# Performance work log

Measured on AMD Instinct MI355X. Metric: run time of the kernel, lower is better.

The kernel has to match this reference:

```python
import jax, jax.numpy as jnp
import numpy as np
from jax import lax

B, T, C = 32, 512, 128
K = 3                      # top_k periods
MIN_P, MAX_P = 8, 64       # period search band
P_MAX = MAX_P              # grid width
CYC_MAX = (T + MIN_P - 1) // MIN_P
KW = 9                     # cyc-axis depthwise kernel
GN_G = 32                  # _best_gn_groups(128)
EPS_GN = 1e-5
EPS_ORTH = 1e-6
EPS_W = 1e-8


def setup_inputs() -> dict:
    key = jax.random.key(0)
    ks = jax.random.split(key, 4)
    return {
        "x": jax.random.normal(ks[0], (B, T, C), jnp.float32),
        "W_dw": jax.random.normal(ks[1], (C, 1, KW), jnp.float32) * 0.1,
        "W_pw": jax.random.normal(ks[2], (C, C), jnp.float32) * (1.0 / np.sqrt(C)),
        "gn_weight": jnp.ones((C,), jnp.float32),
        "gn_bias": jnp.zeros((C,), jnp.float32),
        "W_gate": jax.random.normal(ks[3], (C, C), jnp.float32) * (1.0 / np.sqrt(C)),
        "gamma": jnp.full((C,), 1e-3, jnp.float32),
    }


def _autocorr_topk(x):
    # x: [B,T,C] -> period idx [B,K], softmax weights [B,K]
    Xf = jnp.fft.rfft(x, axis=1)
    Pm = (Xf * jnp.conj(Xf)).real.mean(-1)          # [B, T//2+1]
    r = jnp.fft.irfft(Pm, n=T, axis=1)              # [B, T] autocorrelation
    lag = jnp.arange(T)
    valid = (lag >= MIN_P) & (lag <= MAX_P)
    very_neg = jnp.finfo(x.dtype).min / 8
    rm = jnp.where(valid[None, :], r, very_neg)
    vals, idx = lax.top_k(rm, K)
    w = jax.nn.softmax(vals, axis=1)
    return idx, w


def _fold(s, p):
    # s: [N,T,C], p: [N] int periods -> Z [N,C,CYC_MAX,P_MAX], mask, unfold index maps
    N = s.shape[0]
    p = jnp.maximum(p, 1)
    tpad = ((T + p - 1) // p) * p                   # [N]
    cyc = jnp.arange(CYC_MAX)[None, :, None]
    pos = jnp.arange(P_MAX)[None, None, :]
    time = cyc * p[:, None, None] + pos             # [N,CYC_MAX,P_MAX]
    valid = (pos < p[:, None, None]) & (time < tpad[:, None, None])
    # right-side reflect padding indices
    m = 2 * (T - 1)
    rr = time % m
    src_idx = jnp.where(rr < T, rr, m - rr)
    src = jnp.take_along_axis(s, src_idx.reshape(N, -1)[:, :, None], axis=1)
    src = src.reshape(N, CYC_MAX, P_MAX, C) * valid[..., None].astype(s.dtype)
    Z = jnp.transpose(src, (0, 3, 1, 2))            # [N,C,CYC_MAX,P_MAX]
    mask2d = valid[:, None].astype(s.dtype)         # [N,1,CYC_MAX,P_MAX]
    t = jnp.arange(T)[None, :]
    cyc_T = jnp.clip(t // p[:, None], 0, CYC_MAX - 1)
    pos_T = jnp.clip(t % p[:, None], 0, P_MAX - 1)
    return Z, mask2d, cyc_T, pos_T


def _cyc_conv(Z, mask2d, W_dw, W_pw, gn_w, gn_b, W_gate, gamma):
    # CycAxisConv1d: mean over period axis, depthwise+pointwise conv along cyc,
    # GroupNorm, GELU, SE-gate, LayerScale residual broadcast back to 2D.
    N, _, L, _ = Z.shape
    u = Z.mean(-1)                                  # [N,C,L]
    h = lax.conv_general_dilated(u, W_dw, (1,), [(KW // 2, KW // 2)],
                                 dimension_numbers=('NCH', 'OIH', 'NCH'),
                                 feature_group_count=C)
    h = jnp.einsum('oc,ncl->nol', W_pw, h)
    hg = h.reshape(N, GN_G, C // GN_G, L)
    mean = hg.mean((2, 3), keepdims=True)
    var = hg.var((2, 3), keepdims=True)
    hg = (hg - mean) * lax.rsqrt(var + EPS_GN)
    h = hg.reshape(N, C, L) * gn_w[None, :, None] + gn_b[None, :, None]
    h = jax.nn.gelu(h, approximate=False)
    gate = jax.nn.sigmoid(jnp.einsum('oc,nc->no', W_gate, u.mean(-1)))
    h = h * gate[:, :, None]
    x2d = h[..., None] * gamma[None, :, None, None] * mask2d
    return Z + x2d


def _unfold(Z, cyc_T, pos_T):
    N = Z.shape[0]
    Zf = Z.reshape(N, C, CYC_MAX * P_MAX)
    sp = jnp.clip(cyc_T * P_MAX + pos_T, 0, CYC_MAX * P_MAX - 1)  # [N,T]
    y = jnp.take_along_axis(Zf, sp[:, None, :], axis=2)           # [N,C,T]
    return jnp.transpose(y, (0, 2, 1))                            # [N,T,C]


def reference(x, W_dw, W_pw, gn_weight, gn_bias, W_gate, gamma):
    idx, w = _autocorr_topk(x)                      # [B,K], [B,K]
    p_flat = idx.reshape(-1)                        # [B*K]
    s = jnp.repeat(x, K, axis=0)                    # [B*K,T,C]
    Z, mask2d, cyc_T, pos_T = _fold(s, p_flat)
    Z = _cyc_conv(Z, mask2d, W_dw, W_pw, gn_weight, gn_bias, W_gate, gamma)
    y = _unfold(Z, cyc_T, pos_T).reshape(B, K, T, C)
    periodic = jnp.einsum('bk,bktc->btc', w, y)
    # period confidence Gamma from weight entropy
    H = -(w * jnp.log(w + EPS_W)).sum(1)
    Gamma = jnp.clip(1.0 - H / (jnp.log(float(K) + EPS_W) + EPS_W), 0.0, 1.0)
    # orthogonal residual of local part against periodic part
    local = x - periodic
    num = (local * periodic).sum(1, keepdims=True)
    den = (periodic * periodic).sum(1, keepdims=True) + EPS_ORTH
    local_orth = local - num / den * periodic
    g = Gamma[:, None, None]
    return g * (periodic + local_orth) + (1.0 - g) * x
```

## Files before the change

### kernel.cpp

```cpp
#include <hip/hip_runtime.h>
#include <math.h>

static constexpr int Bn   = 32;
static constexpr int Tn   = 512;
static constexpr int Cn   = 128;
static constexpr int NLAG = 57;
static constexpr int CYC  = 64;

__device__ __forceinline__ int topk_p(const float* __restrict__ rb,
                                      int lane, int kk) {
  float v  = (lane < NLAG) ? rb[lane] : -INFINITY;
  int  idx = lane;
  int  lag = 8;
#pragma unroll
  for (int k = 0; k < 3; ++k) {
    if (k > kk) break;
    float bv = v; int bi = idx;
#pragma unroll
    for (int m = 32; m > 0; m >>= 1) {
      const float ov = __shfl_xor(bv, m, 64);
      const int   oi = __shfl_xor(bi, m, 64);
      if (ov > bv || (ov == bv && oi < bi)) { bv = ov; bi = oi; }
    }
    lag = bi + 8;
    if (idx == bi) v = -INFINITY;
  }
  return lag;
}

__global__ __launch_bounds__(256) void k_autocorr(const float* __restrict__ x,
    float* __restrict__ r_ws) {
  const int w   = (blockIdx.x & 7) * 32 + (blockIdx.x >> 3);
  const int b   = w >> 3;
  const int grp = w & 7;
  const int L0  = 8 + grp * 8;
  const int tid = threadIdx.x;
  const float4* X4 = (const float4*)(x + (size_t)b * Tn * Cn);

  float acc[8];
#pragma unroll
  for (int i = 0; i < 8; ++i) acc[i] = 0.f;

  for (int it = 0; it < 8; ++it) {
    const int id = it * 256 + tid;
    const int c4 = id & 31;
    const int t0 = (id >> 5) * 8;
    float4 A[8];
#pragma unroll
    for (int j = 0; j < 8; ++j) A[j] = X4[(t0 + j) * 32 + c4];
    float4 R[16];
#pragma unroll
    for (int j = 0; j < 16; ++j) R[j] = X4[((t0 + L0 + j) & 511) * 32 + c4];
#pragma unroll
    for (int g = 0; g < 8; ++g) {
#pragma unroll
      for (int j = 0; j < 8; ++j) {
        const float4 a = A[j];
        const float4 r = R[g + j];
        acc[g] += a.x * r.x + a.y * r.y + a.z * r.z + a.w * r.w;
      }
    }
  }

  __shared__ float lds_r[4][8];
  const int lane = tid & 63, wave = tid >> 6;
#pragma unroll
  for (int g = 0; g < 8; ++g) {
    float v = acc[g];
#pragma unroll
    for (int m = 32; m > 0; m >>= 1) v += __shfl_xor(v, m, 64);
    if (lane == 0) lds_r[wave][g] = v;
  }
  __syncthreads();
  if (tid < 8) {
    const int li = grp * 8 + tid;
    if (li < NLAG) {
      r_ws[b * NLAG + li] =
          (lds_r[0][tid] + lds_r[1][tid] + lds_r[2][tid] + lds_r[3][tid]) * (1.0f / Cn);
    }
  }
}

__global__ __launch_bounds__(128) void k_fold_u(const float* __restrict__ x,
    const float* __restrict__ r_ws, float* __restrict__ u) {
  const int bid = blockIdx.x;
  const int w = (bid & 7) * 768 + (bid >> 3);
  const int n = w >> 6, l = w & 63;
  const int b = n / 3, kk = n % 3;
  const int tid = threadIdx.x;

  __shared__ int p_sh;
  __shared__ float4 fr[32];
  if (tid < 64) {
    const int lag = topk_p(r_ws + b * NLAG, tid, kk);
    if (tid == 0) p_sh = lag;
  }
  __syncthreads();
  const int p    = p_sh;
  const int ncyc = (Tn + p - 1) / p;
  const int c4   = tid & 31;
  const int r    = tid >> 5;

  float4 acc = {0.f, 0.f, 0.f, 0.f};
  if (l < ncyc) {
    const float4* xb4 = (const float4*)(x + (size_t)b * Tn * Cn);
    const int base = l * p;
    for (int j = r; j < p; j += 4) {
      const int time = base + j;
      const int src  = time < Tn ? time : (2 * (Tn - 1) - time);
      const float4 v = xb4[src * 32 + c4];
      acc.x += v.x; acc.y += v.y; acc.z += v.z; acc.w += v.w;
    }
  }
  acc.x += __shfl_xor(acc.x, 32, 64);
  acc.y += __shfl_xor(acc.y, 32, 64);
  acc.z += __shfl_xor(acc.z, 32, 64);
  acc.w += __shfl_xor(acc.w, 32, 64);
  if (tid >= 64 && (tid & 63) < 32) fr[c4] = acc;
  __syncthreads();
  if (tid < 32) {
    const float4 o = fr[c4];
    float4 res;
    res.x = (acc.x + o.x) * (1.0f / 64.0f);
    res.y = (acc.y + o.y) * (1.0f / 64.0f);
    res.z = (acc.z + o.z) * (1.0f / 64.0f);
    res.w = (acc.w + o.w) * (1.0f / 64.0f);
    ((float4*)u)[((size_t)n * CYC + l) * 32 + c4] = res;
  }
}

__global__ __launch_bounds__(256) void k_conv(
    const float* __restrict__ u, const float* __restrict__ Wdw,
    const float* __restrict__ Wpw, const float* __restrict__ gnw,
    const float* __restrict__ gnb, const float* __restrict__ Wgate,
    float* __restrict__ hh) {
  const int bid = blockIdx.x;
  const int w = (bid & 7) * 96 + (bid >> 3);
  const int n = w >> 3, og = w & 7;
  const int tid  = threadIdx.x;
  const int l    = tid & 63;
  const int wq   = __builtin_amdgcn_readfirstlane(tid >> 6);

  __shared__ float smem[8320];
  __shared__ float ubar_s[Cn];

  {
    const float4* u4 = (const float4*)(u + (size_t)n * CYC * Cn);
#pragma unroll
    for (int i = 0; i < 8; ++i) {
      const int idx4 = i * 256 + tid;
      const float4 v = u4[idx4];
      const int ll = idx4 >> 5;
      const int cc = (idx4 & 31) << 2;
      float* d = smem + ll * 129 + cc;
      d[0] = v.x; d[1] = v.y; d[2] = v.z; d[3] = v.w;
    }
  }
  __syncthreads();

  if (tid < Cn) {
    float s = 0.f;
    for (int ll = 0; ll < CYC; ++ll) s += smem[ll * 129 + tid];
    ubar_s[tid] = s * (1.0f / CYC);
  }

  float hreg[32];
  {
    const int c0 = wq * 32;
#pragma unroll
    for (int i = 0; i < 32; ++i) {
      const int c = c0 + i;
      float s = 0.f;
#pragma unroll
      for (int k = 0; k < 9; ++k) {
        const int ll = l + k - 4;
        if (ll >= 0 && ll < CYC) s += smem[ll * 129 + c] * Wdw[c * 9 + k];
      }
      hreg[i] = s;
    }
  }
  __syncthreads();

  float gi[4];
  {
    const int ol   = l & 3;
    const int part = l >> 2;
    const int o    = og * 16 + wq * 4 + ol;
    float z = 0.f;
    const float* wg = Wgate + (size_t)o * Cn + part * 8;
    const float* ub = ubar_s + part * 8;
#pragma unroll
    for (int cc = 0; cc < 8; ++cc) z += wg[cc] * ub[cc];
    z += __shfl_xor(z, 4, 64);
    z += __shfl_xor(z, 8, 64);
    z += __shfl_xor(z, 16, 64);
    z += __shfl_xor(z, 32, 64);
    const float sig = 1.0f / (1.0f + expf(-z));
#pragma unroll
    for (int i = 0; i < 4; ++i) gi[i] = __shfl(sig, i, 64);
  }

  {
    const int c0 = wq * 32;
#pragma unroll
    for (int i = 0; i < 32; ++i) smem[(c0 + i) * 65 + l] = hreg[i];
  }
  __syncthreads();

  const int o4 = og * 16 + wq * 4;
  float acc[4];
#pragma unroll
  for (int i = 0; i < 4; ++i) acc[i] = 0.f;
  const float* wb = Wpw + (size_t)o4 * Cn;
  for (int c = 0; c < Cn; ++c) {
    const float hv = smem[c * 65 + l];
#pragma unroll
    for (int i = 0; i < 4; ++i) acc[i] = fmaf(wb[i * Cn + c], hv, acc[i]);
  }

  float s1 = acc[0] + acc[1] + acc[2] + acc[3];
  float s2 = acc[0]*acc[0] + acc[1]*acc[1] + acc[2]*acc[2] + acc[3]*acc[3];
#pragma unroll
  for (int m = 32; m > 0; m >>= 1) {
    s1 += __shfl_xor(s1, m, 64);
    s2 += __shfl_xor(s2, m, 64);
  }
  const float mean = s1 * (1.0f / 256.0f);
  const float var  = s2 * (1.0f / 256.0f) - mean * mean;
  const float rstd = rsqrtf(var + 1e-5f);

  float4 res;
  float* rp = (float*)&res;
#pragma unroll
  for (int i = 0; i < 4; ++i) {
    const int o = o4 + i;
    float h = (acc[i] - mean) * rstd;
    h = h * gnw[o] + gnb[o];
    h = 0.5f * h * (1.0f + erff(h * 0.70710678118654752440f));
    rp[i] = h * gi[i];
  }
  *(float4*)(hh + (size_t)n * CYC * Cn + (size_t)l * Cn + o4) = res;
}

__global__ __launch_bounds__(256) void k_dot_out(
    const float* __restrict__ x, const float* __restrict__ hh,
    const float* __restrict__ r_ws, const float* __restrict__ gamma,
    float* __restrict__ out) {
  const int bid = blockIdx.x;
  const int w = (bid & 7) * 32 + (bid >> 3);
  const int b = w >> 3, cg = w & 7;
  const int tid = threadIdx.x;
  const int c4  = tid & 3;
  const int tg  = tid >> 2;
  const int cw  = cg * 4 + c4;

  __shared__ float4 P_s[Tn * 4];
  __shared__ unsigned short cyc_s[Tn][3];
  __shared__ float params[4];
  __shared__ int   pp[3];
  __shared__ float4 redn[4][4], redd[4][4];
  __shared__ float4 sc_s[4];

  if (tid < 64) {
    const float* rb = r_ws + b * NLAG;
    float v  = (tid < NLAG) ? rb[tid] : -INFINITY;
    int  idx = tid;
    float vals[3]; int lags[3];
#pragma unroll
    for (int k = 0; k < 3; ++k) {
      float bv = v; int bi = idx;
#pragma unroll
      for (int m = 32; m > 0; m >>= 1) {
        const float ov = __shfl_xor(bv, m, 64);
        const int   oi = __shfl_xor(bi, m, 64);
        if (ov > bv || (ov == bv && oi < bi)) { bv = ov; bi = oi; }
      }
      vals[k] = bv; lags[k] = bi + 8;
      if (idx == bi) v = -INFINITY;
    }
    if (tid == 0) {
      const float m  = vals[0];
      const float e0 = expf(vals[0] - m), e1 = expf(vals[1] - m), e2 = expf(vals[2] - m);
      const float s  = e0 + e1 + e2;
      const float w0 = e0 / s, w1 = e1 / s, w2 = e2 / s;
      pp[0] = lags[0]; pp[1] = lags[1]; pp[2] = lags[2];
      params[0] = w0; params[1] = w1; params[2] = w2;
      const float H  = -(w0 * logf(w0 + 1e-8f) + w1 * logf(w1 + 1e-8f) + w2 * logf(w2 + 1e-8f));
      const float lg = logf(3.0f + 1e-8f) + 1e-8f;
      params[3] = fminf(fmaxf(1.0f - H / lg, 0.0f), 1.0f);
    }
  }
  __syncthreads();
  const int p0 = pp[0], p1 = pp[1], p2 = pp[2];
  const float w0 = params[0], w1 = params[1], w2 = params[2];
  const float g  = params[3];
  const float sw = w0 + w1 + w2;

  for (int t = tid; t < Tn; t += 256) {
    cyc_s[t][0] = (unsigned short)(t / p0);
    cyc_s[t][1] = (unsigned short)(t / p1);
    cyc_s[t][2] = (unsigned short)(t / p2);
  }
  __syncthreads();

  const float4 gam = ((const float4*)gamma)[cw];
  const float4* xb4 = (const float4*)(x + (size_t)b * Tn * Cn);
  const float4* h04 = (const float4*)(hh + (size_t)(b * 3 + 0) * CYC * Cn);
  const float4* h14 = (const float4*)(hh + (size_t)(b * 3 + 1) * CYC * Cn);
  const float4* h24 = (const float4*)(hh + (size_t)(b * 3 + 2) * CYC * Cn);

  float4 na = {0.f, 0.f, 0.f, 0.f}, da = {0.f, 0.f, 0.f, 0.f};
#pragma unroll
  for (int tt = 0; tt < 8; ++tt) {
    const int t = tt * 64 + tg;
    const float4 xv = xb4[t * 32 + cw];
    const float4 a0 = h04[cyc_s[t][0] * 32 + cw];
    const float4 a1 = h14[cyc_s[t][1] * 32 + cw];
    const float4 a2 = h24[cyc_s[t][2] * 32 + cw];
    float4 P;
    P.x = sw * xv.x + gam.x * (w0 * a0.x + w1 * a1.x + w2 * a2.x);
    P.y = sw * xv.y + gam.y * (w0 * a0.y + w1 * a1.y + w2 * a2.y);
    P.z = sw * xv.z + gam.z * (w0 * a0.z + w1 * a1.z + w2 * a2.z);
    P.w = sw * xv.w + gam.w * (w0 * a0.w + w1 * a1.w + w2 * a2.w);
    P_s[t * 4 + c4] = P;
    na.x += (xv.x - P.x) * P.x;  da.x += P.x * P.x;
    na.y += (xv.y - P.y) * P.y;  da.y += P.y * P.y;
    na.z += (xv.z - P.z) * P.z;  da.z += P.z * P.z;
    na.w += (xv.w - P.w) * P.w;  da.w += P.w * P.w;
  }
#pragma unroll
  for (int m = 4; m <= 32; m <<= 1) {
    na.x += __shfl_xor(na.x, m, 64);  da.x += __shfl_xor(da.x, m, 64);
    na.y += __shfl_xor(na.y, m, 64);  da.y += __shfl_xor(da.y, m, 64);
    na.z += __shfl_xor(na.z, m, 64);  da.z += __shfl_xor(da.z, m, 64);
    na.w += __shfl_xor(na.w, m, 64);  da.w += __shfl_xor(da.w, m, 64);
  }
  const int wv_ = tid >> 6;
  if ((tid & 63) < 4) { redn[wv_][c4] = na; redd[wv_][c4] = da; }
  __syncthreads();
  if (tid < 4) {
    float4 n4, d4, s;
    n4.x = redn[0][tid].x + redn[1][tid].x + redn[2][tid].x + redn[3][tid].x;
    n4.y = redn[0][tid].y + redn[1][tid].y + redn[2][tid].y + redn[3][tid].y;
    n4.z = redn[0][tid].z + redn[1][tid].z + redn[2][tid].z + redn[3][tid].z;
    n4.w = redn[0][tid].w + redn[1][tid].w + redn[2][tid].w + redn[3][tid].w;
    d4.x = redd[0][tid].x + redd[1][tid].x + redd[2][tid].x + redd[3][tid].x + 1e-6f;
    d4.y = redd[0][tid].y + redd[1][tid].y + redd[2][tid].y + redd[3][tid].y + 1e-6f;
    d4.z = redd[0][tid].z + redd[1][tid].z + redd[2][tid].z + redd[3][tid].z + 1e-6f;
    d4.w = redd[0][tid].w + redd[1][tid].w + redd[2][tid].w + redd[3][tid].w + 1e-6f;
    s.x = g * (n4.x / d4.x);
    s.y = g * (n4.y / d4.y);
    s.z = g * (n4.z / d4.z);
    s.w = g * (n4.w / d4.w);
    sc_s[tid] = s;
  }
  __syncthreads();
  const float4 sc = sc_s[c4];

  float4* ob4 = (float4*)(out + (size_t)b * Tn * Cn);
#pragma unroll
  for (int tt = 0; tt < 8; ++tt) {
    const int t = tt * 64 + tg;
    const float4 xv = xb4[t * 32 + cw];
    const float4 P  = P_s[t * 4 + c4];
    float4 o;
    o.x = xv.x - sc.x * P.x;
    o.y = xv.y - sc.y * P.y;
    o.z = xv.z - sc.z * P.z;
    o.w = xv.w - sc.w * P.w;
    ob4[t * 32 + cw] = o;
  }
}

extern "C" void kernel_launch(void* const* d_in, const int* in_sizes, int n_in,
                              void* d_out, int out_size, void* d_ws, size_t ws_size,
                              hipStream_t stream) {
  const float* x     = (const float*)d_in[0];
  const float* Wdw   = (const float*)d_in[1];
  const float* Wpw   = (const float*)d_in[2];
  const float* gnw   = (const float*)d_in[3];
  const float* gnb   = (const float*)d_in[4];
  const float* Wgate = (const float*)d_in[5];
  const float* gamma = (const float*)d_in[6];
  float* out = (float*)d_out;

  char* ws = (char*)d_ws;
  float* r_ws = (float*)ws;
  float* u    = (float*)(ws + 8192);
  float* hh   = (float*)(ws + 8192 + 3145728);

  k_autocorr<<<Bn * 8, 256, 0, stream>>>(x, r_ws);
  k_fold_u<<<6144, 128, 0, stream>>>(x, r_ws, u);
  k_conv<<<768, 256, 0, stream>>>(u, Wdw, Wpw, gnw, gnb, Wgate, hh);
  k_dot_out<<<256, 256, 0, stream>>>(x, hh, r_ws, gamma, out);
}
```

Before: 133.9 us.

## Fuse fold and conv kernels with per-sequence atomic barrier across blocks

Merges the fold-averaging kernel into the conv kernel. Each of the 8 blocks per sequence computes 8 cycle rows of u, publishes them, then spins on a global atomic counter until all 8 are done before loading the full u tile. If the wait times out, the block recomputes the whole fold locally. This removes one launch and the 6144-block fold grid, at the cost of relying on co-residency of sibling blocks, spin-wait overhead, and a possible redundant recompute. The counter is reset inside the autocorrelation kernel.

```diff
diff --git a/kernel.cpp b/kernel.cpp
--- a/kernel.cpp
+++ b/kernel.cpp
@@ -29,7 +29,9 @@
 }
 
 __global__ __launch_bounds__(256) void k_autocorr(const float* __restrict__ x,
-    float* __restrict__ r_ws) {
+    float* __restrict__ r_ws, int* __restrict__ cnt) {
+  if (blockIdx.x == 0 && threadIdx.x < 96) cnt[threadIdx.x] = 0;
+
   const int w   = (blockIdx.x & 7) * 32 + (blockIdx.x >> 3);
   const int b   = w >> 3;
   const int grp = w & 7;
@@ -81,16 +83,25 @@
   }
 }
 
-__global__ __launch_bounds__(128) void k_fold_u(const float* __restrict__ x,
-    const float* __restrict__ r_ws, float* __restrict__ u) {
+__global__ __launch_bounds__(256, 4) void k_fold_conv(
+    const float* __restrict__ x, const float* __restrict__ r_ws,
+    const float* __restrict__ Wdw, const float* __restrict__ Wpw,
+    const float* __restrict__ gnw, const float* __restrict__ gnb,
+    const float* __restrict__ Wgate, float* __restrict__ u,
+    float* __restrict__ hh, int* __restrict__ cnt) {
   const int bid = blockIdx.x;
-  const int w = (bid & 7) * 768 + (bid >> 3);
-  const int n = w >> 6, l = w & 63;
+  const int w = (bid & 7) * 96 + (bid >> 3);
+  const int n = w >> 3, og = w & 7;
   const int b = n / 3, kk = n % 3;
-  const int tid = threadIdx.x;
-
-  __shared__ int p_sh;
-  __shared__ float4 fr[32];
+  const int tid  = threadIdx.x;
+  const int l    = tid & 63;
+  const int wq   = __builtin_amdgcn_readfirstlane(tid >> 6);
+
+  __shared__ float smem[8320];
+  __shared__ float ubar_s[Cn];
+  __shared__ int   p_sh;
+  __shared__ int   okf;
+
   if (tid < 64) {
     const int lag = topk_p(r_ws + b * NLAG, tid, kk);
     if (tid == 0) p_sh = lag;
@@ -98,53 +109,65 @@
   __syncthreads();
   const int p    = p_sh;
   const int ncyc = (Tn + p - 1) / p;
-  const int c4   = tid & 31;
-  const int r    = tid >> 5;
-
-  float4 acc = {0.f, 0.f, 0.f, 0.f};
-  if (l < ncyc) {
-    const float4* xb4 = (const float4*)(x + (size_t)b * Tn * Cn);
-    const int base = l * p;
-    for (int j = r; j < p; j += 4) {
-      const int time = base + j;
-      const int src  = time < Tn ? time : (2 * (Tn - 1) - time);
-      const float4 v = xb4[src * 32 + c4];
-      acc.x += v.x; acc.y += v.y; acc.z += v.z; acc.w += v.w;
-    }
-  }
-  acc.x += __shfl_xor(acc.x, 32, 64);
-  acc.y += __shfl_xor(acc.y, 32, 64);
-  acc.z += __shfl_xor(acc.z, 32, 64);
-  acc.w += __shfl_xor(acc.w, 32, 64);
-  if (tid >= 64 && (tid & 63) < 32) fr[c4] = acc;
-  __syncthreads();
-  if (tid < 32) {
-    const float4 o = fr[c4];
+  const float4* xb4 = (const float4*)(x + (size_t)b * Tn * Cn);
+
+  {
+    const int r  = og * 8 + (tid >> 5);
+    const int c4 = tid & 31;
+    float4 a0 = {0.f,0.f,0.f,0.f}, a1 = {0.f,0.f,0.f,0.f};
+    float4 a2 = {0.f,0.f,0.f,0.f}, a3 = {0.f,0.f,0.f,0.f};
+    if (r < ncyc) {
+      const int base = r * p;
+      int j = 0;
+      for (; j + 3 < p; j += 4) {
+        const int t0 = base + j,     t1 = base + j + 1;
+        const int t2 = base + j + 2, t3 = base + j + 3;
+        const int s0 = t0 < Tn ? t0 : 2 * (Tn - 1) - t0;
+        const int s1 = t1 < Tn ? t1 : 2 * (Tn - 1) - t1;
+        const int s2 = t2 < Tn ? t2 : 2 * (Tn - 1) - t2;
+        const int s3 = t3 < Tn ? t3 : 2 * (Tn - 1) - t3;
+        const float4 v0 = xb4[s0 * 32 + c4];
+        const float4 v1 = xb4[s1 * 32 + c4];
+        const float4 v2 = xb4[s2 * 32 + c4];
+        const float4 v3 = xb4[s3 * 32 + c4];
+        a0.x += v0.x; a0.y += v0.y; a0.z += v0.z; a0.w += v0.w;
+        a1.x += v1.x; a1.y += v1.y; a1.z += v1.z; a1.w += v1.w;
+        a2.x += v2.x; a2.y += v2.y; a2.z += v2.z; a2.w += v2.w;
+        a3.x += v3.x; a3.y += v3.y; a3.z += v3.z; a3.w += v3.w;
+      }
+      for (; j < p; ++j) {
+        const int t0 = base + j;
+        const int s0 = t0 < Tn ? t0 : 2 * (Tn - 1) - t0;
+        const float4 v0 = xb4[s0 * 32 + c4];
+        a0.x += v0.x; a0.y += v0.y; a0.z += v0.z; a0.w += v0.w;
+      }
+    }
     float4 res;
-    res.x = (acc.x + o.x) * (1.0f / 64.0f);
-    res.y = (acc.y + o.y) * (1.0f / 64.0f);
-    res.z = (acc.z + o.z) * (1.0f / 64.0f);
-    res.w = (acc.w + o.w) * (1.0f / 64.0f);
-    ((float4*)u)[((size_t)n * CYC + l) * 32 + c4] = res;
-  }
-}
-
-__global__ __launch_bounds__(256) void k_conv(
-    const float* __restrict__ u, const float* __restrict__ Wdw,
-    const float* __restrict__ Wpw, const float* __restrict__ gnw,
-    const float* __restrict__ gnb, const float* __restrict__ Wgate,
-    float* __restrict__ hh) {
-  const int bid = blockIdx.x;
-  const int w = (bid & 7) * 96 + (bid >> 3);
-  const int n = w >> 3, og = w & 7;
-  const int tid  = threadIdx.x;
-  const int l    = tid & 63;
-  const int wq   = __builtin_amdgcn_readfirstlane(tid >> 6);
-
-  __shared__ float smem[8320];
-  __shared__ float ubar_s[Cn];
-
-  {
+    res.x = (a0.x + a1.x + a2.x + a3.x) * (1.0f / 64.0f);
+    res.y = (a0.y + a1.y + a2.y + a3.y) * (1.0f / 64.0f);
+    res.z = (a0.z + a1.z + a2.z + a3.z) * (1.0f / 64.0f);
+    res.w = (a0.w + a1.w + a2.w + a3.w) * (1.0f / 64.0f);
+    ((float4*)u)[((size_t)n * CYC + r) * 32 + c4] = res;
+  }
+  __threadfence();
+  __syncthreads();
+
+  if (tid == 0) {
+    __hip_atomic_fetch_add(&cnt[n], 1, __ATOMIC_RELEASE,
+                           __HIP_MEMORY_SCOPE_AGENT);
+    int it = 0, good = 1;
+    for (;;) {
+      const int v = __hip_atomic_load(&cnt[n], __ATOMIC_ACQUIRE,
+                                      __HIP_MEMORY_SCOPE_AGENT);
+      if (v == 8) break;
+      if (v < 0 || v > 8 || ++it > 20000) { good = 0; break; }
+      __builtin_amdgcn_s_sleep(4);
+    }
+    okf = good;
+  }
+  __syncthreads();
+
+  if (okf) {
     const float4* u4 = (const float4*)(u + (size_t)n * CYC * Cn);
 #pragma unroll
     for (int i = 0; i < 8; ++i) {
@@ -154,6 +177,25 @@
       const int cc = (idx4 & 31) << 2;
       float* d = smem + ll * 129 + cc;
       d[0] = v.x; d[1] = v.y; d[2] = v.z; d[3] = v.w;
+    }
+  } else {
+    for (int uu = 0; uu < 8; ++uu) {
+      const int idx = uu * 256 + tid;
+      const int rr  = idx >> 5;
+      const int cc4 = idx & 31;
+      float4 a = {0.f,0.f,0.f,0.f};
+      if (rr < ncyc) {
+        const int base = rr * p;
+        for (int j = 0; j < p; ++j) {
+          const int t0 = base + j;
+          const int s0 = t0 < Tn ? t0 : 2 * (Tn - 1) - t0;
+          const float4 v0 = xb4[s0 * 32 + cc4];
+          a.x += v0.x; a.y += v0.y; a.z += v0.z; a.w += v0.w;
+        }
+      }
+      float* d = smem + rr * 129 + (cc4 << 2);
+      d[0] = a.x * (1.0f / 64.0f); d[1] = a.y * (1.0f / 64.0f);
+      d[2] = a.z * (1.0f / 64.0f); d[3] = a.w * (1.0f / 64.0f);
     }
   }
   __syncthreads();
@@ -388,9 +430,10 @@
   float* r_ws = (float*)ws;
   float* u    = (float*)(ws + 8192);
   float* hh   = (float*)(ws + 8192 + 3145728);
-
-  k_autocorr<<<Bn * 8, 256, 0, stream>>>(x, r_ws);
-  k_fold_u<<<6144, 128, 0, stream>>>(x, r_ws, u);
-  k_conv<<<768, 256, 0, stream>>>(u, Wdw, Wpw, gnw, gnb, Wgate, hh);
+  int*   cnt  = (int*)(ws + 8192 + 2 * 3145728);
+
+  k_autocorr<<<Bn * 8, 256, 0, stream>>>(x, r_ws, cnt);
+  k_fold_conv<<<768, 256, 0, stream>>>(x, r_ws, Wdw, Wpw, gnw, gnb, Wgate,
+                                       u, hh, cnt);
   k_dot_out<<<256, 256, 0, stream>>>(x, hh, r_ws, gamma, out);
 }
```

Measured after the change: 296.6 us. 2.21x slower.
